# Kernel tuning notes

Hardware: AMD Instinct MI355X
Metric: run time of the kernel (lower is better)

The kernel has to match this reference:

```python
import jax, jax.numpy as jnp
import numpy as np
import math

B, C, H, W = 8, 384, 14, 14
HEADS = 12
HC = C // HEADS
STRIDE = 2
K = 3
FACTOR = 2.0
rH = -(-H // STRIDE)
rW = -(-W // STRIDE)
N = H * W
S = rH * rW
KK = K * K
OFFSET_MAT = np.array([[0, -1], [-1, -1], [-1, 0], [-1, 1], [0, 1], [1, 1], [1, 0], [1, -1], [0, 0]], dtype=np.float32)


def bilinear_sample(img, coords):
    """img (Hi,Wi,C); coords (...,2) normalized (y,x) in [-1,1].
    Matches F.grid_sample(mode='bilinear', align_corners=True, padding_mode='zeros')."""
    Hi, Wi = img.shape[0], img.shape[1]
    py = (coords[..., 0] + 1.0) * 0.5 * (Hi - 1)
    px = (coords[..., 1] + 1.0) * 0.5 * (Wi - 1)
    y0 = jnp.floor(py)
    x0 = jnp.floor(px)
    wy1 = py - y0
    wx1 = px - x0

    def corner(yf, xf, wgt):
        valid = (yf >= 0) & (yf <= Hi - 1) & (xf >= 0) & (xf <= Wi - 1)
        yi = jnp.clip(yf, 0, Hi - 1).astype(jnp.int32)
        xi = jnp.clip(xf, 0, Wi - 1).astype(jnp.int32)
        return img[yi, xi] * (wgt * valid)[..., None]

    return (corner(y0, x0, (1 - wy1) * (1 - wx1)) + corner(y0, x0 + 1, (1 - wy1) * wx1)
            + corner(y0 + 1, x0, wy1 * (1 - wx1)) + corner(y0 + 1, x0 + 1, wy1 * wx1))


def _forward(x, Wq, bq, Wk, bk, Wv, bv, Wo1, bo1, Wdw, bdw, ln_g, ln_b, Wo2, Wco, posembed, Wp, bp):
    dt = x.dtype
    xh = jnp.transpose(x, (0, 2, 3, 1))                       # B,H,W,C
    q = jnp.einsum('bhwc,oc->bhwo', xh, Wq) + bq              # q_conv (1x1)

    # ---- offset network: 1x1 conv -> GELU -> 3x3 dw stride conv -> LN -> GELU -> 1x1 ----
    t = jax.nn.gelu(jnp.einsum('bhwc,oc->bhwo', q, Wo1) + bo1, approximate=False)
    ker = jnp.transpose(Wdw, (2, 3, 1, 0))                    # (3,3,1,C) for HWIO depthwise
    t = jax.lax.conv_general_dilated(t, ker, (STRIDE, STRIDE), ((1, 1), (1, 1)),
                                     dimension_numbers=('NHWC', 'HWIO', 'NHWC'),
                                     feature_group_count=C) + bdw  # B,rH,rW,C
    mu = t.mean(-1, keepdims=True)
    var = ((t - mu) ** 2).mean(-1, keepdims=True)
    t = (t - mu) / jnp.sqrt(var + 1e-5) * ln_g + ln_b
    t = jax.nn.gelu(t, approximate=False)
    off = jnp.einsum('bhwc,oc->bhwo', t, Wo2)                 # B,rH,rW,2*N ; channel = (g,h,w)
    off = off.reshape(B, rH, rW, 2, N)
    off = jnp.transpose(off, (0, 3, 4, 1, 2))                 # B,2,N,rH,rW
    ranges = jnp.array([1.0 / H, 1.0 / W], dtype=dt)
    off = jnp.tanh(off) * ranges[None, :, None, None, None] * FACTOR
    off = jnp.transpose(off, (0, 2, 3, 4, 1))                 # B,N,rH,rW,2 (y,x)

    # ---- strided reference grid + deformable bilinear gather from x ----
    gy = jnp.arange(0, H, STRIDE, dtype=dt) / (H - 1) * 2 - 1
    gx = jnp.arange(0, W, STRIDE, dtype=dt) / (W - 1) * 2 - 1
    ref = jnp.stack(jnp.meshgrid(gy, gx, indexing='ij'), -1)  # rH,rW,2
    dpos = off + ref
    sampled = jax.vmap(bilinear_sample)(xh, dpos).reshape(B, N, S, C)

    # ---- k x k center points with learned offsets ----
    cy = jnp.arange(H, dtype=dt)
    cx = jnp.arange(W, dtype=dt)
    center = jnp.stack(jnp.meshgrid(cy, cx, indexing='ij'), -1).reshape(N, 1, 2)
    offmat = jnp.asarray(OFFSET_MAT, dtype=dt)
    cpt = center + offmat[None]                               # N,KK,2
    cpt_norm = jnp.stack([jnp.clip(cpt[..., 0], 0, H) / (H - 1) * 2 - 1,
                          jnp.clip(cpt[..., 1], 0, W) / (W - 1) * 2 - 1], -1).reshape(N, K, K, 2)
    q_tok = q.reshape(B, N, C)
    co = jnp.tanh(jnp.einsum('bnc,oc->bno', q_tok, Wco).reshape(B, N, K, K, 2)) * ranges
    cgrid = co + cpt_norm[None]
    csampled = jax.vmap(bilinear_sample)(xh, cgrid).reshape(B, N, KK, C)

    feats = jnp.concatenate([sampled, csampled], axis=2)      # B,N,S+KK,C
    k = (jnp.einsum('bnsc,oc->bnso', feats, Wk) + bk).reshape(B, N, S + KK, HEADS, HC)
    v = (jnp.einsum('bnsc,oc->bnso', feats, Wv) + bv).reshape(B, N, S + KK, HEADS, HC)
    qh = q_tok.reshape(B, N, HEADS, HC)
    attn = jnp.einsum('bnhd,bnshd->bhns', qh, k)              # qk_scale=None -> no scaling

    # ---- dynamic relative position bias (grid_sample into rel-pos table) ----
    a = jnp.arange(0, H, STRIDE, dtype=dt)
    bcol = jnp.arange(0, W, dtype=dt)
    ref_pos = a[None, :] - bcol[:, None]                      # (W, rH)
    ref_pos_x = jnp.tile(ref_pos, (H, rH))                    # (N, S)
    ref_pos_y = jnp.repeat(jnp.repeat(ref_pos, W, axis=0), rW, axis=1)
    rpp = jnp.stack([ref_pos_y / (H - 1), ref_pos_x / (W - 1)], -1)  # N,S,2
    rel = rpp.reshape(N, rH, rW, 2)[None] - off               # B,N,rH,rW,2
    table = jnp.transpose(posembed, (1, 2, 0))                # (2H-1, 2W-1, heads)
    d_rel = bilinear_sample(table, rel).reshape(B, N, S, HEADS)
    cpt_raw = jnp.broadcast_to(center, (N, KK, 2)).reshape(N, K, K, 2)
    crel = co - cpt_raw[None]
    d_crel = bilinear_sample(table, crel).reshape(B, N, KK, HEADS)
    bias = jnp.concatenate([d_rel, d_crel], axis=2)           # B,N,S+KK,heads
    attn = attn + jnp.transpose(bias, (0, 3, 1, 2))
    attn = jax.nn.softmax(attn, axis=-1)

    out = jnp.einsum('bhns,bnshd->bnhd', attn, v).reshape(B, N, C)
    out = jnp.einsum('bnc,oc->bno', out, Wp) + bp             # proj (1x1)
    return jnp.transpose(out.reshape(B, H, W, C), (0, 3, 1, 2))


def setup_inputs() -> dict:
    key = jax.random.key(0)
    ks = jax.random.split(key, 20)
    def w(k, shape, s=0.05):
        return jax.random.normal(k, shape, dtype=jnp.float32) * s
    return {
        'x': jax.random.normal(ks[0], (B, C, H, W), dtype=jnp.float32),
        'Wq': w(ks[1], (C, C)), 'bq': w(ks[2], (C,)),
        'Wk': w(ks[3], (C, C)), 'bk': w(ks[4], (C,)),
        'Wv': w(ks[5], (C, C)), 'bv': w(ks[6], (C,)),
        'Wo1': w(ks[7], (C, C)), 'bo1': w(ks[8], (C,)),
        'Wdw': w(ks[9], (C, 1, 3, 3), 0.2), 'bdw': w(ks[10], (C,)),
        'ln_g': jnp.ones((C,), jnp.float32), 'ln_b': jnp.zeros((C,), jnp.float32),
        'Wo2': w(ks[11], (2 * N, C)),
        'Wco': w(ks[12], (2 * K * K, C)),
        'posembed': w(ks[13], (HEADS, 2 * H - 1, 2 * W - 1), 0.02),
        'Wp': w(ks[14], (C, C)), 'bp': w(ks[15], (C,)),
    }


def reference(x, Wq, bq, Wk, bk, Wv, bv, Wo1, bo1, Wdw, bdw, ln_g, ln_b, Wo2, Wco, posembed, Wp, bp):
    return _forward(x, Wq, bq, Wk, bk, Wv, bv, Wo1, bo1, Wdw, bdw, ln_g, ln_b, Wo2, Wco, posembed, Wp, bp)
```

## Files before the change

kernel.cpp:

```cpp
#include <hip/hip_runtime.h>
#include <hip/hip_bf16.h>
#include <math.h>

#define BB 8
#define CC 384
#define HH 14
#define WW 14
#define NHEADS 12
#define RH 7
#define RW 7
#define NN 196
#define SS 49
#define KKK 9
#define SK 58
#define TH 27
#define NTOK 1568

typedef float    f4 __attribute__((ext_vector_type(4)));
typedef _Float16 h8 __attribute__((ext_vector_type(8)));
typedef _Float16 h4 __attribute__((ext_vector_type(4)));

__device__ __forceinline__ float geluf(float x){ return 0.5f*x*(1.0f+erff(x*0.7071067811865475f)); }
__device__ __forceinline__ f4 mfma16h(h8 a, h8 b, f4 c){
  return __builtin_amdgcn_mfma_f32_16x16x32_f16(a, b, c, 0, 0, 0);
}

__constant__ float c_offm[9][2] = {{0,-1},{-1,-1},{-1,0},{-1,1},{0,1},{1,1},{1,0},{1,-1},{0,0}};

__global__ void __launch_bounds__(256) k_transpose2(const float* __restrict__ x,
                                                    float* __restrict__ xh, _Float16* __restrict__ xhh){
  __shared__ float tile[48*203];
  int b = blockIdx.x >> 3, c0 = (blockIdx.x & 7)*48;
  int t = threadIdx.x;
  for (int i = t; i < 48*49; i += 256){
    int row = i / 49, seg = i % 49;
    f4 v = *(const f4*)(x + ((size_t)(b*CC + c0 + row))*NN + seg*4);
    #pragma unroll
    for (int j = 0; j < 4; ++j) tile[row*203 + seg*4 + j] = v[j];
  }
  __syncthreads();
  for (int i = t; i < 196*12; i += 256){
    int n = i / 12, seg = i % 12;
    f4 v; h4 vh;
    #pragma unroll
    for (int j = 0; j < 4; ++j){ v[j] = tile[(seg*4 + j)*203 + n]; vh[j] = (_Float16)v[j]; }
    size_t o = ((size_t)(b*NN + n))*CC + c0 + seg*4;
    *(f4*)(xh + o) = v;
    *(h4*)(xhh + o) = vh;
  }
}

__device__ __forceinline__ void gemm_hilo_body(
    const float* __restrict__ A, const float* __restrict__ W,
    int arow, int brow, _Float16* sbuf, int t, f4 acc[4]){
  _Float16* Ah = sbuf; _Float16* Al = sbuf + 2560;
  _Float16* Bh = sbuf + 5120; _Float16* Bl = sbuf + 7680;
  int w = t>>6, lane = t&63, col = lane&15, quad = lane>>4;
  int r = t>>2, cg = t&3;
  const float* Ar = A + (size_t)arow*384 + cg*8;
  const float* Br = W + (size_t)brow*384 + cg*8;
  f4 a0 = *(const f4*)(Ar),     a1 = *(const f4*)(Ar + 4);
  f4 b0 = *(const f4*)(Br),     b1 = *(const f4*)(Br + 4);
  for (int k0 = 0; k0 < 384; k0 += 32){
    h8 ah, al, bh, bl;
    #pragma unroll
    for (int j = 0; j < 4; ++j){
      ah[j] = (_Float16)a0[j];   al[j] = (_Float16)(a0[j] - (float)ah[j]);
      ah[4+j] = (_Float16)a1[j]; al[4+j] = (_Float16)(a1[j] - (float)ah[4+j]);
      bh[j] = (_Float16)b0[j];   bl[j] = (_Float16)(b0[j] - (float)bh[j]);
      bh[4+j] = (_Float16)b1[j]; bl[4+j] = (_Float16)(b1[j] - (float)bh[4+j]);
    }
    __syncthreads();
    *(h8*)(Ah + r*40 + cg*8) = ah; *(h8*)(Al + r*40 + cg*8) = al;
    *(h8*)(Bh + r*40 + cg*8) = bh; *(h8*)(Bl + r*40 + cg*8) = bl;
    __syncthreads();
    if (k0 < 352){
      a0 = *(const f4*)(Ar + k0 + 32); a1 = *(const f4*)(Ar + k0 + 36);
      b0 = *(const f4*)(Br + k0 + 32); b1 = *(const f4*)(Br + k0 + 36);
    }
    h8 afh = *(const h8*)(Ah + (w*16+col)*40 + quad*8);
    h8 afl = *(const h8*)(Al + (w*16+col)*40 + quad*8);
    #pragma unroll
    for (int nt = 0; nt < 4; ++nt){
      h8 bfh = *(const h8*)(Bh + (nt*16+col)*40 + quad*8);
      h8 bfl = *(const h8*)(Bl + (nt*16+col)*40 + quad*8);
      acc[nt] = mfma16h(afh, bfh, acc[nt]);
      acc[nt] = mfma16h(afl, bfh, acc[nt]);
      acc[nt] = mfma16h(afh, bfl, acc[nt]);
    }
  }
}

template<int EPI>
__global__ void __launch_bounds__(256) k_mmf(const float* __restrict__ A, const float* __restrict__ W,
                                             const float* __restrict__ bias, float* __restrict__ out,
                                             _Float16* __restrict__ out16, int M, int N){
  __shared__ __align__(16) _Float16 sbuf[10240];
  int t = threadIdx.x;
  int w = t>>6, lane = t&63, col = lane&15, quad = lane>>4;
  int m0 = blockIdx.x*64, n0 = blockIdx.y*64;
  int r = t>>2;
  int arow = min(m0 + r, M-1);
  int brow = min(n0 + r, N-1);
  f4 acc[4] = {{0,0,0,0},{0,0,0,0},{0,0,0,0},{0,0,0,0}};
  gemm_hilo_body(A, W, arow, brow, sbuf, t, acc);
  if constexpr (EPI == 2){
    float* tile = (float*)sbuf;
    __syncthreads();
    #pragma unroll
    for (int nt = 0; nt < 4; ++nt)
      #pragma unroll
      for (int rr = 0; rr < 4; ++rr)
        tile[(w*16 + quad*4 + rr)*65 + nt*16 + col] = acc[nt][rr];
    __syncthreads();
    for (int i = t; i < 1024; i += 256){
      int o_l = i >> 4, ms = i & 15;
      int m = m0 + ms*4;
      if (m >= M) continue;
      int bb = m / NN, nnn = m % NN;
      int o = n0 + o_l;
      float bo = bias[o];
      f4 v = { tile[(ms*4+0)*65 + o_l] + bo, tile[(ms*4+1)*65 + o_l] + bo,
               tile[(ms*4+2)*65 + o_l] + bo, tile[(ms*4+3)*65 + o_l] + bo };
      *(f4*)(out + ((size_t)bb*384 + o)*NN + nnn) = v;
    }
  } else {
    #pragma unroll
    for (int nt = 0; nt < 4; ++nt){
      #pragma unroll
      for (int rr = 0; rr < 4; ++rr){
        int m = m0 + w*16 + quad*4 + rr;
        int o = n0 + nt*16 + col;
        if (m >= M || o >= N) continue;
        float v = acc[nt][rr] + bias[o];
        if (EPI == 1) v = geluf(v);
        out[(size_t)m*384 + o] = v;
      }
    }
  }
}

__global__ void __launch_bounds__(256) k_qkv(
    const float* __restrict__ xh, const _Float16* __restrict__ xhh,
    const float* __restrict__ Wq, const float* __restrict__ bq,
    const float* __restrict__ Wk, const float* __restrict__ Wv,
    float* __restrict__ qf, _Float16* __restrict__ K2h, _Float16* __restrict__ VprojT){
  __shared__ __align__(16) _Float16 sbuf[10240];
  int t = threadIdx.x;
  int w = t>>6, lane = t&63, col = lane&15, quad = lane>>4;
  int bid = blockIdx.x;

  if (bid < 300){
    int isK = (bid >= 150) ? 1 : 0;
    int r2 = isK ? bid - 150 : bid;
    const float* W = isK ? Wk : Wq;
    int m0 = (r2/6)*64, n0 = (r2%6)*64;
    int r = t>>2;
    int arow = min(m0 + r, NTOK-1);
    int brow = n0 + r;
    f4 acc[4] = {{0,0,0,0},{0,0,0,0},{0,0,0,0},{0,0,0,0}};
    gemm_hilo_body(xh, W, arow, brow, sbuf, t, acc);
    #pragma unroll
    for (int nt = 0; nt < 4; ++nt){
      #pragma unroll
      for (int rr = 0; rr < 4; ++rr){
        int m = m0 + w*16 + quad*4 + rr;
        int o = n0 + nt*16 + col;
        if (m >= NTOK) continue;
        if (isK){
          K2h[(size_t)m*384 + o] = (_Float16)acc[nt][rr];
        } else {
          qf[(size_t)m*384 + o] = acc[nt][rr] + bq[o];
        }
      }
    }
  } else {
    int idx = bid - 300;
    int mo = idx % 6;
    int ny = (idx / 6) % 4;
    int b  = idx / 24;
    int m0 = mo*64, n0 = ny*64;
    int orow = m0 + w*16 + col;
    const float* wvr = Wv + (size_t)orow*384;
    f4 acc[4] = {{0,0,0,0},{0,0,0,0},{0,0,0,0},{0,0,0,0}};
    for (int kt = 0; kt < 12; ++kt){
      f4 a0 = *(const f4*)(wvr + kt*32 + quad*8);
      f4 a1 = *(const f4*)(wvr + kt*32 + quad*8 + 4);
      h8 ah, al;
      #pragma unroll
      for (int j = 0; j < 4; ++j){
        ah[j] = (_Float16)a0[j];   al[j] = (_Float16)(a0[j] - (float)ah[j]);
        ah[4+j] = (_Float16)a1[j]; al[4+j] = (_Float16)(a1[j] - (float)ah[4+j]);
      }
      #pragma unroll
      for (int nt = 0; nt < 4; ++nt){
        int i = min(n0 + nt*16 + col, 195);
        h8 b8 = *(const h8*)(xhh + ((size_t)(b*196 + i))*384 + kt*32 + quad*8);
        acc[nt] = mfma16h(ah, b8, acc[nt]);
        acc[nt] = mfma16h(al, b8, acc[nt]);
      }
    }
    #pragma unroll
    for (int nt = 0; nt < 4; ++nt){
      #pragma unroll
      for (int rr = 0; rr < 4; ++rr){
        int o = m0 + w*16 + quad*4 + rr;
        int i = n0 + nt*16 + col;
        if (i < 224)
          VprojT[((size_t)(b*384 + o))*224 + i] = (i < 196) ? (_Float16)acc[nt][rr] : (_Float16)0.f;
      }
    }
  }
}

__global__ void __launch_bounds__(384) k_dwln(const float* __restrict__ t1,
      const float* __restrict__ Wdw, const float* __restrict__ bdw,
      const float* __restrict__ lng, const float* __restrict__ lnb,
      float* __restrict__ t2){
  int blk = blockIdx.x;
  int ow = blk % RW; int oh = (blk / RW) % RH; int b = blk / (RH*RW);
  int c = threadIdx.x;
  float acc = bdw[c];
  #pragma unroll
  for (int kh = 0; kh < 3; ++kh){
    int ih = oh*2 - 1 + kh;
    if (ih < 0 || ih >= HH) continue;
    #pragma unroll
    for (int kw = 0; kw < 3; ++kw){
      int iw = ow*2 - 1 + kw;
      if (iw < 0 || iw >= WW) continue;
      acc += t1[((b*HH + ih)*WW + iw)*CC + c] * Wdw[c*9 + kh*3 + kw];
    }
  }
  __shared__ float red[6];
  __shared__ float s_mu, s_rv;
  float v = acc;
  #pragma unroll
  for (int o = 32; o > 0; o >>= 1) v += __shfl_down(v, o);
  int wid = c >> 6, lane = c & 63;
  if (lane == 0) red[wid] = v;
  __syncthreads();
  if (c == 0){ float s = 0.f; for (int i = 0; i < 6; ++i) s += red[i]; s_mu = s / CC; }
  __syncthreads();
  float mu = s_mu;
  float d = acc - mu;
  v = d*d;
  #pragma unroll
  for (int o = 32; o > 0; o >>= 1) v += __shfl_down(v, o);
  if (lane == 0) red[wid] = v;
  __syncthreads();
  if (c == 0){ float s = 0.f; for (int i = 0; i < 6; ++i) s += red[i]; s_rv = rsqrtf(s / CC + 1e-5f); }
  __syncthreads();
  float val = d * s_rv * lng[c] + lnb[c];
  t2[blk*CC + c] = geluf(val);
}

__global__ void __launch_bounds__(256) k_off(const float* __restrict__ t2, const float* __restrict__ Wo2,
                                             float* __restrict__ offp){
  __shared__ __align__(16) _Float16 sbuf[10240];
  int t = threadIdx.x;
  int w = t>>6, lane = t&63, col = lane&15, quad = lane>>4;
  int bid = blockIdx.x;
  int m0 = (bid/7)*64, n0 = (bid%7)*64;
  int r = t>>2;
  int arow = min(m0 + r, 391);
  int brow = min(n0 + r, 391);
  f4 acc[4] = {{0,0,0,0},{0,0,0,0},{0,0,0,0},{0,0,0,0}};
  gemm_hilo_body(t2, Wo2, arow, brow, sbuf, t, acc);
  #pragma unroll
  for (int nt = 0; nt < 4; ++nt){
    #pragma unroll
    for (int rr = 0; rr < 4; ++rr){
      int row = m0 + w*16 + quad*4 + rr;
      int o = n0 + nt*16 + col;
      if (row < 392 && o < 392){
        int g = o / NN, nn = o % NN;
        int b = row / SS, s = row % SS;
        float rng = (g == 0) ? (1.0f/HH) : (1.0f/WW);
        offp[((b*NN + nn)*SS + s)*2 + g] = tanhf(acc[nt][rr]) * rng * 2.0f;
      }
    }
  }
}

__global__ void __launch_bounds__(256) k_mid(const float* __restrict__ qf, const float* __restrict__ Wo1,
                                             const float* __restrict__ bo1, float* __restrict__ t1,
                                             const _Float16* __restrict__ K2h, _Float16* __restrict__ G16){
  __shared__ __align__(16) _Float16 sbuf[10240];
  int t = threadIdx.x;
  int w = t>>6, lane = t&63, col = lane&15, quad = lane>>4;
  int bid = blockIdx.x;
  if (bid < 150){
    int m0 = (bid/6)*64, n0 = (bid%6)*64;
    int r = t>>2;
    int arow = min(m0 + r, NTOK-1);
    int brow = n0 + r;
    f4 acc[4] = {{0,0,0,0},{0,0,0,0},{0,0,0,0},{0,0,0,0}};
    gemm_hilo_body(qf, Wo1, arow, brow, sbuf, t, acc);
    #pragma unroll
    for (int nt = 0; nt < 4; ++nt){
      #pragma unroll
      for (int rr = 0; rr < 4; ++rr){
        int m = m0 + w*16 + quad*4 + rr;
        int o = n0 + nt*16 + col;
        if (m >= NTOK) continue;
        t1[(size_t)m*384 + o] = geluf(acc[nt][rr] + bo1[o]);
      }
    }
  } else {
    int idx = bid - 150;
    int m0 = (idx & 3)*64;
    int bh = idx >> 2; int b = bh / 12, h = bh - b*12;
    const float* qr = qf + ((size_t)(b*196 + min(m0 + w*16 + col, 195)))*384 + h*32;
    f4 q0 = *(const f4*)(qr + quad*8);
    f4 q1 = *(const f4*)(qr + quad*8 + 4);
    h8 a8;
    #pragma unroll
    for (int j = 0; j < 4; ++j){ a8[j] = (_Float16)q0[j]; a8[4+j] = (_Float16)q1[j]; }
    f4 acc[13];
    #pragma unroll
    for (int nt = 0; nt < 13; ++nt){
      int i = min(nt*16 + col, 195);
      h8 b8 = *(const h8*)(K2h + ((size_t)(b*196 + i))*384 + h*32 + quad*8);
      f4 z = {0.f,0.f,0.f,0.f};
      acc[nt] = mfma16h(a8, b8, z);
    }
    #pragma unroll
    for (int nt = 0; nt < 13; ++nt){
      #pragma unroll
      for (int r = 0; r < 4; ++r){
        int m = m0 + w*16 + quad*4 + r;
        int i = nt*16 + col;
        if (m < 196 && i < 196)
          G16[((size_t)(b*196 + m))*2352 + h*196 + i] = (_Float16)acc[nt][r];
      }
    }
  }
}

__global__ void __launch_bounds__(256, 7) k_fused(
    const float* __restrict__ qf, const float* __restrict__ off,
    const _Float16* __restrict__ G16,
    const float* __restrict__ bk, const float* __restrict__ Wco, const float* __restrict__ pos,
    _Float16* __restrict__ agg16){
  __shared__ __align__(16) _Float16 Gs[2352];
  __shared__ __align__(16) float agg[12*228];
  __shared__ float scoreS[696];
  __shared__ float offl[98];
  __shared__ float colb[18];
  __shared__ float qbv[12];
  __shared__ uint2 tapv[232];
  float* qrow = agg;

  int blk = blockIdx.x;
  int n = blk % NN, b = blk / NN;
  int iy = n / WW, ix = n % WW;
  int t = threadIdx.x;

  {
    const h8* g8 = (const h8*)(G16 + (size_t)blk*2352);
    h8* gs8 = (h8*)Gs;
    for (int i = t; i < 294; i += 256) gs8[i] = g8[i];
  }
  {
    const f4* q4 = (const f4*)(qf + (size_t)blk*384);
    f4* qr4 = (f4*)qrow;
    for (int i = t; i < 96; i += 256) qr4[i] = q4[i];
  }
  for (int i = t; i < 98; i += 256) offl[i] = off[(size_t)blk*98 + i];
  __syncthreads();

  if (t < 144){
    int o = t >> 3, l = t & 7;
    const float* wr = Wco + o*384 + l*48;
    const float* qr = qrow + l*48;
    f4 a4 = {0.f,0.f,0.f,0.f};
    #pragma unroll
    for (int c = 0; c < 48; c += 4) a4 += (*(const f4*)(qr + c)) * (*(const f4*)(wr + c));
    float acc = a4[0]+a4[1]+a4[2]+a4[3];
    acc += __shfl_xor(acc, 1); acc += __shfl_xor(acc, 2); acc += __shfl_xor(acc, 4);
    if (l == 0){
      int g = o & 1;
      float range = (g == 0) ? (1.0f/HH) : (1.0f/WW);
      colb[o] = tanhf(acc) * range;
    }
  }
  if (t >= 160){
    int o = t - 160;
    int h = o >> 3, l = o & 7;
    float acc = 0.f;
    for (int d = l; d < 32; d += 8) acc += qrow[h*32 + d] * bk[h*32 + d];
    acc += __shfl_xor(acc, 1); acc += __shfl_xor(acc, 2); acc += __shfl_xor(acc, 4);
    if (l == 0 && h < 12) qbv[h] = acc;
  }
  __syncthreads();

  if (t < SK){
    float cy, cx;
    if (t < SS){
      int sy = t / RW, sx = t % RW;
      cy = offl[t*2+0] + ((2.0f*sy)/13.0f*2.0f - 1.0f);
      cx = offl[t*2+1] + ((2.0f*sx)/13.0f*2.0f - 1.0f);
    } else {
      int kk = t - SS;
      float cyr = fminf(fmaxf((float)iy + c_offm[kk][0], 0.f), (float)HH);
      float cxr = fminf(fmaxf((float)ix + c_offm[kk][1], 0.f), (float)WW);
      cy = colb[kk*2+0] + (cyr/13.0f*2.0f - 1.0f);
      cx = colb[kk*2+1] + (cxr/13.0f*2.0f - 1.0f);
    }
    float py = (cy + 1.0f)*0.5f*13.0f;
    float px = (cx + 1.0f)*0.5f*13.0f;
    float y0 = floorf(py), x0 = floorf(px);
    float wy1 = py - y0, wx1 = px - x0;
    #pragma unroll
    for (int k4 = 0; k4 < 4; ++k4){
      float yf = y0 + (k4 >> 1), xf = x0 + (k4 & 1);
      bool valid = (yf >= 0.f) && (yf <= 13.f) && (xf >= 0.f) && (xf <= 13.f);
      int yi = (int)fminf(fmaxf(yf, 0.f), 13.f);
      int xi = (int)fminf(fmaxf(xf, 0.f), 13.f);
      float wgt = ((k4 >> 1) ? wy1 : (1.f - wy1)) * ((k4 & 1) ? wx1 : (1.f - wx1));
      tapv[t*4 + k4] = make_uint2(__float_as_uint(valid ? wgt : 0.f),
                                  (unsigned)(yi*WW + xi));
    }
  }
  __syncthreads();
  for (int i = t; i < 12*228; i += 256) agg[i] = 0.f;

  if (t < 232){
    int s = t >> 2, grp = t & 3;
    float ry, rx;
    if (s < SS){
      int sy = s / RW, sx = s % RW;
      ry = (2.0f*sy - iy)/13.0f - offl[s*2+0];
      rx = (2.0f*sx - ix)/13.0f - offl[s*2+1];
    } else {
      int kk = s - SS;
      ry = colb[kk*2+0] - (float)iy;
      rx = colb[kk*2+1] - (float)ix;
    }
    float py = (ry + 1.0f)*0.5f*26.0f;
    float px = (rx + 1.0f)*0.5f*26.0f;
    float y0 = floorf(py), x0 = floorf(px);
    float wy1 = py - y0, wx1 = px - x0;
    int pidx[4]; float pw[4];
    #pragma unroll
    for (int k4 = 0; k4 < 4; ++k4){
      float yf = y0 + (k4 >> 1), xf = x0 + (k4 & 1);
      bool valid = (yf >= 0.f) && (yf <= 26.f) && (xf >= 0.f) && (xf <= 26.f);
      int yi = (int)fminf(fmaxf(yf, 0.f), 26.f);
      int xi = (int)fminf(fmaxf(xf, 0.f), 26.f);
      pidx[k4] = yi*TH + xi;
      float wgt = ((k4 >> 1) ? wy1 : (1.f - wy1)) * ((k4 & 1) ? wx1 : (1.f - wx1));
      pw[k4] = valid ? wgt : 0.f;
    }
    uint2 tp0 = tapv[s*4+0], tp1 = tapv[s*4+1], tp2 = tapv[s*4+2], tp3 = tapv[s*4+3];
    float tw0 = __uint_as_float(tp0.x), tw1 = __uint_as_float(tp1.x);
    float tw2 = __uint_as_float(tp2.x), tw3 = __uint_as_float(tp3.x);
    #pragma unroll
    for (int hh = 0; hh < 3; ++hh){
      int h = grp*3 + hh;
      const float* pt = pos + h*729;
      float val = qbv[h];
      val += pt[pidx[0]]*pw[0];
      val += pt[pidx[1]]*pw[1];
      val += pt[pidx[2]]*pw[2];
      val += pt[pidx[3]]*pw[3];
      const _Float16* gh = Gs + h*196;
      val += tw0*(float)gh[(int)tp0.y];
      val += tw1*(float)gh[(int)tp1.y];
      val += tw2*(float)gh[(int)tp2.y];
      val += tw3*(float)gh[(int)tp3.y];
      scoreS[h*58 + s] = val;
    }
  }
  __syncthreads();

  if (t < 192){
    int h = t >> 4, l = t & 15;
    float v[4];
    #pragma unroll
    for (int k = 0; k < 4; ++k){ int s = l + 16*k; v[k] = (s < SK) ? scoreS[h*58 + s] : -1e30f; }
    float mx = fmaxf(fmaxf(v[0], v[1]), fmaxf(v[2], v[3]));
    mx = fmaxf(mx, __shfl_xor(mx, 1)); mx = fmaxf(mx, __shfl_xor(mx, 2));
    mx = fmaxf(mx, __shfl_xor(mx, 4)); mx = fmaxf(mx, __shfl_xor(mx, 8));
    float e[4], sum = 0.f;
    #pragma unroll
    for (int k = 0; k < 4; ++k){ int s = l + 16*k; e[k] = (s < SK) ? expf(v[k] - mx) : 0.f; sum += e[k]; }
    sum += __shfl_xor(sum, 1); sum += __shfl_xor(sum, 2);
    sum += __shfl_xor(sum, 4); sum += __shfl_xor(sum, 8);
    float inv = 1.0f / sum;
    #pragma unroll
    for (int k = 0; k < 4; ++k){
      int s = l + 16*k;
      if (s < SK) scoreS[h*58 + s] = e[k]*inv;
    }
  }
  __syncthreads();

  if (t < 232){
    uint2 tp = tapv[t];
    float wv = __uint_as_float(tp.x);
    if (wv != 0.f){
      int s = t >> 2, cell = (int)tp.y;
      float* ag = agg + cell;
      #pragma unroll
      for (int h = 0; h < 12; ++h)
        atomicAdd(ag + h*228, scoreS[h*58 + s]*wv);
    }
  }
  __syncthreads();

  {
    _Float16* ar = agg16 + (size_t)blk*2688;
    for (int i = t; i < 336; i += 256){
      int d = i*8;
      int h = d / 224, j = d - h*224;
      const float* src = agg + h*228 + j;
      f4 a = *(const f4*)src;
      f4 c = *(const f4*)(src + 4);
      h8 o;
      #pragma unroll
      for (int k = 0; k < 4; ++k){ o[k] = (_Float16)a[k]; o[4+k] = (_Float16)c[k]; }
      *(h8*)(ar + d) = o;
    }
  }
}

__global__ void __launch_bounds__(256) k_av(const _Float16* __restrict__ agg16,
                                            const _Float16* __restrict__ VprojT,
                                            const float* __restrict__ bv, float* __restrict__ otok){
  int t = threadIdx.x;
  int w = t>>6, lane = t&63, col = lane&15, quad = lane>>4;
  int m0 = blockIdx.x*64;
  int bh = blockIdx.y; int b = bh / 12, h = bh - b*12;
  const _Float16* ar = agg16 + ((size_t)(b*196 + min(m0 + w*16 + col, 195)))*2688 + h*224;
  f4 acc[2] = {{0,0,0,0},{0,0,0,0}};
  for (int kt = 0; kt < 7; ++kt){
    h8 a8 = *(const h8*)(ar + kt*32 + quad*8);
    #pragma unroll
    for (int nt = 0; nt < 2; ++nt){
      int o = h*32 + nt*16 + col;
      h8 b8 = *(const h8*)(VprojT + ((size_t)(b*384 + o))*224 + kt*32 + quad*8);
      acc[nt] = mfma16h(a8, b8, acc[nt]);
    }
  }
  #pragma unroll
  for (int nt = 0; nt < 2; ++nt){
    #pragma unroll
    for (int rr = 0; rr < 4; ++rr){
      int m = m0 + w*16 + quad*4 + rr;
      if (m < 196){
        int o = h*32 + nt*16 + col;
        otok[((size_t)(b*196 + m))*384 + o] = acc[nt][rr] + bv[o];
      }
    }
  }
}

extern "C" void kernel_launch(void* const* d_in, const int* in_sizes, int n_in,
                              void* d_out, int out_size, void* d_ws, size_t ws_size,
                              hipStream_t stream){
  const float* x    = (const float*)d_in[0];
  const float* Wq   = (const float*)d_in[1];
  const float* bq   = (const float*)d_in[2];
  const float* Wk   = (const float*)d_in[3];
  const float* bk   = (const float*)d_in[4];
  const float* Wv   = (const float*)d_in[5];
  const float* bv   = (const float*)d_in[6];
  const float* Wo1  = (const float*)d_in[7];
  const float* bo1  = (const float*)d_in[8];
  const float* Wdw  = (const float*)d_in[9];
  const float* bdw  = (const float*)d_in[10];
  const float* ln_g = (const float*)d_in[11];
  const float* ln_b = (const float*)d_in[12];
  const float* Wo2  = (const float*)d_in[13];
  const float* Wco  = (const float*)d_in[14];
  const float* pos  = (const float*)d_in[15];
  const float* Wp   = (const float*)d_in[16];
  const float* bp   = (const float*)d_in[17];
  float* out = (float*)d_out;

  float* ws   = (float*)d_ws;
  float* xh   = ws;
  float* qf   = xh   + 602112;
  float* t1   = qf   + 602112;
  float* t2   = t1   + 602112;
  float* offp = t2   + 150528;
  float* otok = offp + 153664;
  _Float16* xhh    = (_Float16*)(otok + 602112);
  _Float16* K2h    = xhh    + 602112;
  _Float16* VprojT = K2h    + 602112;
  _Float16* G16    = VprojT + 688128;
  _Float16* agg16  = G16    + 3687936;

  k_transpose2<<<64, 256, 0, stream>>>(x, xh, xhh);
  k_qkv<<<492, 256, 0, stream>>>(xh, xhh, Wq, bq, Wk, Wv, qf, K2h, VprojT);
  k_mid<<<534, 256, 0, stream>>>(qf, Wo1, bo1, t1, K2h, G16);
  k_dwln<<<392, 384, 0, stream>>>(t1, Wdw, bdw, ln_g, ln_b, t2);
  k_off<<<49, 256, 0, stream>>>(t2, Wo2, offp);
  k_fused<<<1568, 256, 0, stream>>>(qf, offp, G16, bk, Wco, pos, agg16);
  k_av<<<dim3(4,96), 256, 0, stream>>>(agg16, VprojT, bv, otok);
  k_mmf<2><<<dim3(25,6), 256, 0, stream>>>(otok, Wp, bp, out, nullptr, NTOK, 384);
}
```

Baseline: 198.3 us.

## Precompute fp16 hi/lo splits of weights and activations once, feed GEMMs directly

After: 194.9 us, median of 2. Within noise of the previous version (-1.7%).

```diff
diff --git a/kernel.cpp b/kernel.cpp
--- a/kernel.cpp
+++ b/kernel.cpp
@@ -15,6 +15,8 @@
 #define SK 58
 #define TH 27
 #define NTOK 1568
+#define WSZ 147456
+#define WO2SZ 150528
 
 typedef float    f4 __attribute__((ext_vector_type(4)));
 typedef _Float16 h8 __attribute__((ext_vector_type(8)));
@@ -27,56 +29,90 @@
 
 __constant__ float c_offm[9][2] = {{0,-1},{-1,-1},{-1,0},{-1,1},{0,1},{1,1},{1,0},{1,-1},{0,0}};
 
-__global__ void __launch_bounds__(256) k_transpose2(const float* __restrict__ x,
-                                                    float* __restrict__ xh, _Float16* __restrict__ xhh){
+__global__ void __launch_bounds__(256) k_pre(const float* __restrict__ x,
+    _Float16* __restrict__ xhh, _Float16* __restrict__ xlo,
+    const float* __restrict__ Wq, const float* __restrict__ Wk, const float* __restrict__ Wo1,
+    const float* __restrict__ Wp, const float* __restrict__ Wv, const float* __restrict__ Wo2,
+    _Float16* __restrict__ Wh, _Float16* __restrict__ Wl){
   __shared__ float tile[48*203];
-  int b = blockIdx.x >> 3, c0 = (blockIdx.x & 7)*48;
+  int bid = blockIdx.x;
   int t = threadIdx.x;
-  for (int i = t; i < 48*49; i += 256){
-    int row = i / 49, seg = i % 49;
-    f4 v = *(const f4*)(x + ((size_t)(b*CC + c0 + row))*NN + seg*4);
-    #pragma unroll
-    for (int j = 0; j < 4; ++j) tile[row*203 + seg*4 + j] = v[j];
-  }
-  __syncthreads();
-  for (int i = t; i < 196*12; i += 256){
-    int n = i / 12, seg = i % 12;
-    f4 v; h4 vh;
-    #pragma unroll
-    for (int j = 0; j < 4; ++j){ v[j] = tile[(seg*4 + j)*203 + n]; vh[j] = (_Float16)v[j]; }
-    size_t o = ((size_t)(b*NN + n))*CC + c0 + seg*4;
-    *(f4*)(xh + o) = v;
-    *(h4*)(xhh + o) = vh;
-  }
-}
-
-__device__ __forceinline__ void gemm_hilo_body(
-    const float* __restrict__ A, const float* __restrict__ W,
+  if (bid < 64){
+    int b = bid >> 3, c0 = (bid & 7)*48;
+    for (int i = t; i < 48*49; i += 256){
+      int row = i / 49, seg = i % 49;
+      f4 v = *(const f4*)(x + ((size_t)(b*CC + c0 + row))*NN + seg*4);
+      #pragma unroll
+      for (int j = 0; j < 4; ++j) tile[row*203 + seg*4 + j] = v[j];
+    }
+    __syncthreads();
+    for (int i = t; i < 196*12; i += 256){
+      int n = i / 12, seg = i % 12;
+      h4 vh, vl;
+      #pragma unroll
+      for (int j = 0; j < 4; ++j){
+        float v = tile[(seg*4 + j)*203 + n];
+        vh[j] = (_Float16)v;
+        vl[j] = (_Float16)(v - (float)vh[j]);
+      }
+      size_t o = ((size_t)(b*NN + n))*CC + c0 + seg*4;
+      *(h4*)(xhh + o) = vh;
+      *(h4*)(xlo + o) = vl;
+    }
+  } else if (bid < 424){
+    int bid2 = bid - 64;
+    int mat = bid2 / 72;
+    int e0 = (bid2 % 72)*2048 + t*8;
+    const float* src = mat==0?Wq: mat==1?Wk: mat==2?Wo1: mat==3?Wp: Wv;
+    f4 v0 = *(const f4*)(src + e0);
+    f4 v1 = *(const f4*)(src + e0 + 4);
+    h8 hi, lo;
+    #pragma unroll
+    for (int j = 0; j < 4; ++j){
+      hi[j]   = (_Float16)v0[j]; lo[j]   = (_Float16)(v0[j] - (float)hi[j]);
+      hi[4+j] = (_Float16)v1[j]; lo[4+j] = (_Float16)(v1[j] - (float)hi[4+j]);
+    }
+    *(h8*)(Wh + (size_t)mat*WSZ + e0) = hi;
+    *(h8*)(Wl + (size_t)mat*WSZ + e0) = lo;
+  } else {
+    int e0 = (bid - 424)*2048 + t*8;
+    if (e0 < WO2SZ){
+      f4 v0 = *(const f4*)(Wo2 + e0);
+      f4 v1 = *(const f4*)(Wo2 + e0 + 4);
+      h8 hi, lo;
+      #pragma unroll
+      for (int j = 0; j < 4; ++j){
+        hi[j]   = (_Float16)v0[j]; lo[j]   = (_Float16)(v0[j] - (float)hi[j]);
+        hi[4+j] = (_Float16)v1[j]; lo[4+j] = (_Float16)(v1[j] - (float)hi[4+j]);
+      }
+      *(h8*)(Wh + (size_t)5*WSZ + e0) = hi;
+      *(h8*)(Wl + (size_t)5*WSZ + e0) = lo;
+    }
+  }
+}
+
+__device__ __forceinline__ void gemm_pre_body(
+    const _Float16* __restrict__ Ahg, const _Float16* __restrict__ Alg,
+    const _Float16* __restrict__ Bhg, const _Float16* __restrict__ Blg,
     int arow, int brow, _Float16* sbuf, int t, f4 acc[4]){
   _Float16* Ah = sbuf; _Float16* Al = sbuf + 2560;
   _Float16* Bh = sbuf + 5120; _Float16* Bl = sbuf + 7680;
   int w = t>>6, lane = t&63, col = lane&15, quad = lane>>4;
   int r = t>>2, cg = t&3;
-  const float* Ar = A + (size_t)arow*384 + cg*8;
-  const float* Br = W + (size_t)brow*384 + cg*8;
-  f4 a0 = *(const f4*)(Ar),     a1 = *(const f4*)(Ar + 4);
-  f4 b0 = *(const f4*)(Br),     b1 = *(const f4*)(Br + 4);
+  const _Float16* Arh = Ahg + (size_t)arow*384 + cg*8;
+  const _Float16* Arl = Alg + (size_t)arow*384 + cg*8;
+  const _Float16* Brh = Bhg + (size_t)brow*384 + cg*8;
+  const _Float16* Brl = Blg + (size_t)brow*384 + cg*8;
+  h8 ah = *(const h8*)(Arh), al = *(const h8*)(Arl);
+  h8 bh = *(const h8*)(Brh), bl = *(const h8*)(Brl);
   for (int k0 = 0; k0 < 384; k0 += 32){
-    h8 ah, al, bh, bl;
-    #pragma unroll
-    for (int j = 0; j < 4; ++j){
-      ah[j] = (_Float16)a0[j];   al[j] = (_Float16)(a0[j] - (float)ah[j]);
-      ah[4+j] = (_Float16)a1[j]; al[4+j] = (_Float16)(a1[j] - (float)ah[4+j]);
-      bh[j] = (_Float16)b0[j];   bl[j] = (_Float16)(b0[j] - (float)bh[j]);
-      bh[4+j] = (_Float16)b1[j]; bl[4+j] = (_Float16)(b1[j] - (float)bh[4+j]);
-    }
     __syncthreads();
     *(h8*)(Ah + r*40 + cg*8) = ah; *(h8*)(Al + r*40 + cg*8) = al;
     *(h8*)(Bh + r*40 + cg*8) = bh; *(h8*)(Bl + r*40 + cg*8) = bl;
     __syncthreads();
     if (k0 < 352){
-      a0 = *(const f4*)(Ar + k0 + 32); a1 = *(const f4*)(Ar + k0 + 36);
-      b0 = *(const f4*)(Br + k0 + 32); b1 = *(const f4*)(Br + k0 + 36);
+      ah = *(const h8*)(Arh + k0 + 32); al = *(const h8*)(Arl + k0 + 32);
+      bh = *(const h8*)(Brh + k0 + 32); bl = *(const h8*)(Brl + k0 + 32);
     }
     h8 afh = *(const h8*)(Ah + (w*16+col)*40 + quad*8);
     h8 afl = *(const h8*)(Al + (w*16+col)*40 + quad*8);
@@ -91,60 +127,12 @@
   }
 }
 
-template<int EPI>
-__global__ void __launch_bounds__(256) k_mmf(const float* __restrict__ A, const float* __restrict__ W,
-                                             const float* __restrict__ bias, float* __restrict__ out,
-                                             _Float16* __restrict__ out16, int M, int N){
-  __shared__ __align__(16) _Float16 sbuf[10240];
-  int t = threadIdx.x;
-  int w = t>>6, lane = t&63, col = lane&15, quad = lane>>4;
-  int m0 = blockIdx.x*64, n0 = blockIdx.y*64;
-  int r = t>>2;
-  int arow = min(m0 + r, M-1);
-  int brow = min(n0 + r, N-1);
-  f4 acc[4] = {{0,0,0,0},{0,0,0,0},{0,0,0,0},{0,0,0,0}};
-  gemm_hilo_body(A, W, arow, brow, sbuf, t, acc);
-  if constexpr (EPI == 2){
-    float* tile = (float*)sbuf;
-    __syncthreads();
-    #pragma unroll
-    for (int nt = 0; nt < 4; ++nt)
-      #pragma unroll
-      for (int rr = 0; rr < 4; ++rr)
-        tile[(w*16 + quad*4 + rr)*65 + nt*16 + col] = acc[nt][rr];
-    __syncthreads();
-    for (int i = t; i < 1024; i += 256){
-      int o_l = i >> 4, ms = i & 15;
-      int m = m0 + ms*4;
-      if (m >= M) continue;
-      int bb = m / NN, nnn = m % NN;
-      int o = n0 + o_l;
-      float bo = bias[o];
-      f4 v = { tile[(ms*4+0)*65 + o_l] + bo, tile[(ms*4+1)*65 + o_l] + bo,
-               tile[(ms*4+2)*65 + o_l] + bo, tile[(ms*4+3)*65 + o_l] + bo };
-      *(f4*)(out + ((size_t)bb*384 + o)*NN + nnn) = v;
-    }
-  } else {
-    #pragma unroll
-    for (int nt = 0; nt < 4; ++nt){
-      #pragma unroll
-      for (int rr = 0; rr < 4; ++rr){
-        int m = m0 + w*16 + quad*4 + rr;
-        int o = n0 + nt*16 + col;
-        if (m >= M || o >= N) continue;
-        float v = acc[nt][rr] + bias[o];
-        if (EPI == 1) v = geluf(v);
-        out[(size_t)m*384 + o] = v;
-      }
-    }
-  }
-}
-
 __global__ void __launch_bounds__(256) k_qkv(
-    const float* __restrict__ xh, const _Float16* __restrict__ xhh,
-    const float* __restrict__ Wq, const float* __restrict__ bq,
-    const float* __restrict__ Wk, const float* __restrict__ Wv,
-    float* __restrict__ qf, _Float16* __restrict__ K2h, _Float16* __restrict__ VprojT){
+    const _Float16* __restrict__ xhh, const _Float16* __restrict__ xlo,
+    const _Float16* __restrict__ Wh, const _Float16* __restrict__ Wl,
+    const float* __restrict__ bq,
+    float* __restrict__ qf, _Float16* __restrict__ qfh, _Float16* __restrict__ qfl,
+    _Float16* __restrict__ K2h, _Float16* __restrict__ VprojT){
   __shared__ __align__(16) _Float16 sbuf[10240];
   int t = threadIdx.x;
   int w = t>>6, lane = t&63, col = lane&15, quad = lane>>4;
@@ -153,13 +141,14 @@
   if (bid < 300){
     int isK = (bid >= 150) ? 1 : 0;
     int r2 = isK ? bid - 150 : bid;
-    const float* W = isK ? Wk : Wq;
+    const _Float16* Bh = Wh + (size_t)(isK ? 1 : 0)*WSZ;
+    const _Float16* Bl = Wl + (size_t)(isK ? 1 : 0)*WSZ;
     int m0 = (r2/6)*64, n0 = (r2%6)*64;
     int r = t>>2;
     int arow = min(m0 + r, NTOK-1);
     int brow = n0 + r;
     f4 acc[4] = {{0,0,0,0},{0,0,0,0},{0,0,0,0},{0,0,0,0}};
-    gemm_hilo_body(xh, W, arow, brow, sbuf, t, acc);
+    gemm_pre_body(xhh, xlo, Bh, Bl, arow, brow, sbuf, t, acc);
     #pragma unroll
     for (int nt = 0; nt < 4; ++nt){
       #pragma unroll
@@ -170,7 +159,11 @@
         if (isK){
           K2h[(size_t)m*384 + o] = (_Float16)acc[nt][rr];
         } else {
-          qf[(size_t)m*384 + o] = acc[nt][rr] + bq[o];
+          float v = acc[nt][rr] + bq[o];
+          qf[(size_t)m*384 + o] = v;
+          _Float16 vh = (_Float16)v;
+          qfh[(size_t)m*384 + o] = vh;
+          qfl[(size_t)m*384 + o] = (_Float16)(v - (float)vh);
         }
       }
     }
@@ -181,17 +174,12 @@
     int b  = idx / 24;
     int m0 = mo*64, n0 = ny*64;
     int orow = m0 + w*16 + col;
-    const float* wvr = Wv + (size_t)orow*384;
+    const _Float16* wvh = Wh + (size_t)4*WSZ + (size_t)orow*384;
+    const _Float16* wvl = Wl + (size_t)4*WSZ + (size_t)orow*384;
     f4 acc[4] = {{0,0,0,0},{0,0,0,0},{0,0,0,0},{0,0,0,0}};
     for (int kt = 0; kt < 12; ++kt){
-      f4 a0 = *(const f4*)(wvr + kt*32 + quad*8);
-      f4 a1 = *(const f4*)(wvr + kt*32 + quad*8 + 4);
-      h8 ah, al;
-      #pragma unroll
-      for (int j = 0; j < 4; ++j){
-        ah[j] = (_Float16)a0[j];   al[j] = (_Float16)(a0[j] - (float)ah[j]);
-        ah[4+j] = (_Float16)a1[j]; al[4+j] = (_Float16)(a1[j] - (float)ah[4+j]);
-      }
+      h8 ah = *(const h8*)(wvh + kt*32 + quad*8);
+      h8 al = *(const h8*)(wvl + kt*32 + quad*8);
       #pragma unroll
       for (int nt = 0; nt < 4; ++nt){
         int i = min(n0 + nt*16 + col, 195);
@@ -213,10 +201,65 @@
   }
 }
 
+__global__ void __launch_bounds__(256) k_mid(
+    const _Float16* __restrict__ qfh, const _Float16* __restrict__ qfl,
+    const _Float16* __restrict__ Wh, const _Float16* __restrict__ Wl,
+    const float* __restrict__ bo1, float* __restrict__ t1,
+    const _Float16* __restrict__ K2h, _Float16* __restrict__ G16){
+  __shared__ __align__(16) _Float16 sbuf[10240];
+  int t = threadIdx.x;
+  int w = t>>6, lane = t&63, col = lane&15, quad = lane>>4;
+  int bid = blockIdx.x;
+  if (bid < 150){
+    const _Float16* Bh = Wh + (size_t)2*WSZ;
+    const _Float16* Bl = Wl + (size_t)2*WSZ;
+    int m0 = (bid/6)*64, n0 = (bid%6)*64;
+    int r = t>>2;
+    int arow = min(m0 + r, NTOK-1);
+    int brow = n0 + r;
+    f4 acc[4] = {{0,0,0,0},{0,0,0,0},{0,0,0,0},{0,0,0,0}};
+    gemm_pre_body(qfh, qfl, Bh, Bl, arow, brow, sbuf, t, acc);
+    #pragma unroll
+    for (int nt = 0; nt < 4; ++nt){
+      #pragma unroll
+      for (int rr = 0; rr < 4; ++rr){
+        int m = m0 + w*16 + quad*4 + rr;
+        int o = n0 + nt*16 + col;
+        if (m >= NTOK) continue;
+        t1[(size_t)m*384 + o] = geluf(acc[nt][rr] + bo1[o]);
+      }
+    }
+  } else {
+    int idx = bid - 150;
+    int m0 = (idx & 3)*64;
+    int bh = idx >> 2; int b = bh / 12, h = bh - b*12;
+    const _Float16* qr = qfh + ((size_t)(b*196 + min(m0 + w*16 + col, 195)))*384 + h*32;
+    h8 a8 = *(const h8*)(qr + quad*8);
+    f4 acc[13];
+    #pragma unroll
+    for (int nt = 0; nt < 13; ++nt){
+      int i = min(nt*16 + col, 195);
+      h8 b8 = *(const h8*)(K2h + ((size_t)(b*196 + i))*384 + h*32 + quad*8);
+      f4 z = {0.f,0.f,0.f,0.f};
+      acc[nt] = mfma16h(a8, b8, z);
+    }
+    #pragma unroll
+    for (int nt = 0; nt < 13; ++nt){
+      #pragma unroll
+      for (int r = 0; r < 4; ++r){
+        int m = m0 + w*16 + quad*4 + r;
+        int i = nt*16 + col;
+        if (m < 196 && i < 196)
+          G16[((size_t)(b*196 + m))*2352 + h*196 + i] = (_Float16)acc[nt][r];
+      }
+    }
+  }
+}
+
 __global__ void __launch_bounds__(384) k_dwln(const float* __restrict__ t1,
       const float* __restrict__ Wdw, const float* __restrict__ bdw,
       const float* __restrict__ lng, const float* __restrict__ lnb,
-      float* __restrict__ t2){
+      _Float16* __restrict__ t2h, _Float16* __restrict__ t2l){
   int blk = blockIdx.x;
   int ow = blk % RW; int oh = (blk / RW) % RH; int b = blk / (RH*RW);
   int c = threadIdx.x;
@@ -251,12 +294,16 @@
   __syncthreads();
   if (c == 0){ float s = 0.f; for (int i = 0; i < 6; ++i) s += red[i]; s_rv = rsqrtf(s / CC + 1e-5f); }
   __syncthreads();
-  float val = d * s_rv * lng[c] + lnb[c];
-  t2[blk*CC + c] = geluf(val);
-}
-
-__global__ void __launch_bounds__(256) k_off(const float* __restrict__ t2, const float* __restrict__ Wo2,
-                                             float* __restrict__ offp){
+  float val = geluf(d * s_rv * lng[c] + lnb[c]);
+  _Float16 vh = (_Float16)val;
+  t2h[blk*CC + c] = vh;
+  t2l[blk*CC + c] = (_Float16)(val - (float)vh);
+}
+
+__global__ void __launch_bounds__(256) k_off(
+    const _Float16* __restrict__ t2h, const _Float16* __restrict__ t2l,
+    const _Float16* __restrict__ Wh, const _Float16* __restrict__ Wl,
+    float* __restrict__ offp){
   __shared__ __align__(16) _Float16 sbuf[10240];
   int t = threadIdx.x;
   int w = t>>6, lane = t&63, col = lane&15, quad = lane>>4;
@@ -265,8 +312,10 @@
   int r = t>>2;
   int arow = min(m0 + r, 391);
   int brow = min(n0 + r, 391);
+  const _Float16* Bh = Wh + (size_t)5*WSZ;
+  const _Float16* Bl = Wl + (size_t)5*WSZ;
   f4 acc[4] = {{0,0,0,0},{0,0,0,0},{0,0,0,0},{0,0,0,0}};
-  gemm_hilo_body(t2, Wo2, arow, brow, sbuf, t, acc);
+  gemm_pre_body(t2h, t2l, Bh, Bl, arow, brow, sbuf, t, acc);
   #pragma unroll
   for (int nt = 0; nt < 4; ++nt){
     #pragma unroll
@@ -278,61 +327,6 @@
         int b = row / SS, s = row % SS;
         float rng = (g == 0) ? (1.0f/HH) : (1.0f/WW);
         offp[((b*NN + nn)*SS + s)*2 + g] = tanhf(acc[nt][rr]) * rng * 2.0f;
-      }
-    }
-  }
-}
-
-__global__ void __launch_bounds__(256) k_mid(const float* __restrict__ qf, const float* __restrict__ Wo1,
-                                             const float* __restrict__ bo1, float* __restrict__ t1,
-                                             const _Float16* __restrict__ K2h, _Float16* __restrict__ G16){
-  __shared__ __align__(16) _Float16 sbuf[10240];
-  int t = threadIdx.x;
-  int w = t>>6, lane = t&63, col = lane&15, quad = lane>>4;
-  int bid = blockIdx.x;
-  if (bid < 150){
-    int m0 = (bid/6)*64, n0 = (bid%6)*64;
-    int r = t>>2;
-    int arow = min(m0 + r, NTOK-1);
-    int brow = n0 + r;
-    f4 acc[4] = {{0,0,0,0},{0,0,0,0},{0,0,0,0},{0,0,0,0}};
-    gemm_hilo_body(qf, Wo1, arow, brow, sbuf, t, acc);
-    #pragma unroll
-    for (int nt = 0; nt < 4; ++nt){
-      #pragma unroll
-      for (int rr = 0; rr < 4; ++rr){
-        int m = m0 + w*16 + quad*4 + rr;
-        int o = n0 + nt*16 + col;
-        if (m >= NTOK) continue;
-        t1[(size_t)m*384 + o] = geluf(acc[nt][rr] + bo1[o]);
-      }
-    }
-  } else {
-    int idx = bid - 150;
-    int m0 = (idx & 3)*64;
-    int bh = idx >> 2; int b = bh / 12, h = bh - b*12;
-    const float* qr = qf + ((size_t)(b*196 + min(m0 + w*16 + col, 195)))*384 + h*32;
-    f4 q0 = *(const f4*)(qr + quad*8);
-    f4 q1 = *(const f4*)(qr + quad*8 + 4);
-    h8 a8;
-    #pragma unroll
-    for (int j = 0; j < 4; ++j){ a8[j] = (_Float16)q0[j]; a8[4+j] = (_Float16)q1[j]; }
-    f4 acc[13];
-    #pragma unroll
-    for (int nt = 0; nt < 13; ++nt){
-      int i = min(nt*16 + col, 195);
-      h8 b8 = *(const h8*)(K2h + ((size_t)(b*196 + i))*384 + h*32 + quad*8);
-      f4 z = {0.f,0.f,0.f,0.f};
-      acc[nt] = mfma16h(a8, b8, z);
-    }
-    #pragma unroll
-    for (int nt = 0; nt < 13; ++nt){
-      #pragma unroll
-      for (int r = 0; r < 4; ++r){
-        int m = m0 + w*16 + quad*4 + r;
-        int i = nt*16 + col;
-        if (m < 196 && i < 196)
-          G16[((size_t)(b*196 + m))*2352 + h*196 + i] = (_Float16)acc[nt][r];
       }
     }
   }
@@ -528,7 +522,8 @@
 
 __global__ void __launch_bounds__(256) k_av(const _Float16* __restrict__ agg16,
                                             const _Float16* __restrict__ VprojT,
-                                            const float* __restrict__ bv, float* __restrict__ otok){
+                                            const float* __restrict__ bv,
+                                            _Float16* __restrict__ otokh, _Float16* __restrict__ otokl){
   int t = threadIdx.x;
   int w = t>>6, lane = t&63, col = lane&15, quad = lane>>4;
   int m0 = blockIdx.x*64;
@@ -551,9 +546,49 @@
       int m = m0 + w*16 + quad*4 + rr;
       if (m < 196){
         int o = h*32 + nt*16 + col;
-        otok[((size_t)(b*196 + m))*384 + o] = acc[nt][rr] + bv[o];
-      }
-    }
+        float v = acc[nt][rr] + bv[o];
+        size_t idx = ((size_t)(b*196 + m))*384 + o;
+        _Float16 vh = (_Float16)v;
+        otokh[idx] = vh;
+        otokl[idx] = (_Float16)(v - (float)vh);
+      }
+    }
+  }
+}
+
+__global__ void __launch_bounds__(256) k_proj(
+    const _Float16* __restrict__ otokh, const _Float16* __restrict__ otokl,
+    const _Float16* __restrict__ Wh, const _Float16* __restrict__ Wl,
+    const float* __restrict__ bias, float* __restrict__ out){
+  __shared__ __align__(16) _Float16 sbuf[10240];
+  int t = threadIdx.x;
+  int w = t>>6, lane = t&63, col = lane&15, quad = lane>>4;
+  int m0 = blockIdx.x*64, n0 = blockIdx.y*64;
+  int r = t>>2;
+  int arow = min(m0 + r, NTOK-1);
+  int brow = n0 + r;
+  const _Float16* Bh = Wh + (size_t)3*WSZ;
+  const _Float16* Bl = Wl + (size_t)3*WSZ;
+  f4 acc[4] = {{0,0,0,0},{0,0,0,0},{0,0,0,0},{0,0,0,0}};
+  gemm_pre_body(otokh, otokl, Bh, Bl, arow, brow, sbuf, t, acc);
+  float* tile = (float*)sbuf;
+  __syncthreads();
+  #pragma unroll
+  for (int nt = 0; nt < 4; ++nt)
+    #pragma unroll
+    for (int rr = 0; rr < 4; ++rr)
+      tile[(w*16 + quad*4 + rr)*65 + nt*16 + col] = acc[nt][rr];
+  __syncthreads();
+  for (int i = t; i < 1024; i += 256){
+    int o_l = i >> 4, ms = i & 15;
+    int m = m0 + ms*4;
+    if (m >= NTOK) continue;
+    int bb = m / NN, nnn = m % NN;
+    int o = n0 + o_l;
+    float bo = bias[o];
+    f4 v = { tile[(ms*4+0)*65 + o_l] + bo, tile[(ms*4+1)*65 + o_l] + bo,
+             tile[(ms*4+2)*65 + o_l] + bo, tile[(ms*4+3)*65 + o_l] + bo };
+    *(f4*)(out + ((size_t)bb*384 + o)*NN + nnn) = v;
   }
 }
 
@@ -581,24 +616,30 @@
   float* out = (float*)d_out;
 
   float* ws   = (float*)d_ws;
-  float* xh   = ws;
-  float* qf   = xh   + 602112;
+  float* qf   = ws;
   float* t1   = qf   + 602112;
-  float* t2   = t1   + 602112;
-  float* offp = t2   + 150528;
-  float* otok = offp + 153664;
-  _Float16* xhh    = (_Float16*)(otok + 602112);
-  _Float16* K2h    = xhh    + 602112;
+  float* offp = t1   + 602112;
+  _Float16* xhh    = (_Float16*)(offp + 153664);
+  _Float16* xlo    = xhh    + 602112;
+  _Float16* qfh    = xlo    + 602112;
+  _Float16* qfl    = qfh    + 602112;
+  _Float16* t2h    = qfl    + 602112;
+  _Float16* t2l    = t2h    + 150528;
+  _Float16* K2h    = t2l    + 150528;
   _Float16* VprojT = K2h    + 602112;
-  _Float16* G16    = VprojT + 688128;
+  _Float16* otokh  = VprojT + 688128;
+  _Float16* otokl  = otokh  + 602112;
+  _Float16* Wh     = otokl  + 602112;
+  _Float16* Wl     = Wh     + 5*WSZ + WO2SZ;
+  _Float16* G16    = Wl     + 5*WSZ + WO2SZ;
   _Float16* agg16  = G16    + 3687936;
 
-  k_transpose2<<<64, 256, 0, stream>>>(x, xh, xhh);
-  k_qkv<<<492, 256, 0, stream>>>(xh, xhh, Wq, bq, Wk, Wv, qf, K2h, VprojT);
-  k_mid<<<534, 256, 0, stream>>>(qf, Wo1, bo1, t1, K2h, G16);
-  k_dwln<<<392, 384, 0, stream>>>(t1, Wdw, bdw, ln_g, ln_b, t2);
-  k_off<<<49, 256, 0, stream>>>(t2, Wo2, offp);
+  k_pre<<<498, 256, 0, stream>>>(x, xhh, xlo, Wq, Wk, Wo1, Wp, Wv, Wo2, Wh, Wl);
+  k_qkv<<<492, 256, 0, stream>>>(xhh, xlo, Wh, Wl, bq, qf, qfh, qfl, K2h, VprojT);
+  k_mid<<<534, 256, 0, stream>>>(qfh, qfl, Wh, Wl, bo1, t1, K2h, G16);
+  k_dwln<<<392, 384, 0, stream>>>(t1, Wdw, bdw, ln_g, ln_b, t2h, t2l);
+  k_off<<<49, 256, 0, stream>>>(t2h, t2l, Wh, Wl, offp);
   k_fused<<<1568, 256, 0, stream>>>(qf, offp, G16, bk, Wco, pos, agg16);
-  k_av<<<dim3(4,96), 256, 0, stream>>>(agg16, VprojT, bv, otok);
-  k_mmf<2><<<dim3(25,6), 256, 0, stream>>>(otok, Wp, bp, out, nullptr, NTOK, 384);
-}
+  k_av<<<dim3(4,96), 256, 0, stream>>>(agg16, VprojT, bv, otokh, otokl);
+  k_proj<<<dim3(25,6), 256, 0, stream>>>(otokh, otokl, Wh, Wl, bp, out);
+}
```
